# Kernel tuning notes

Measured on AMD Instinct MI355X. Metric: run time of the kernel, lower is better.

## Reference

```python
import jax, jax.numpy as jnp
import numpy as np

PH, PW = 7, 7          # output_size
GRID = 2               # sampling_ratio
SCALES = (0.25, 0.125, 0.0625, 0.03125)  # 2^round(log2(feat/img)) per level
LVL_MIN, LVL_MAX = 2, 5                  # -log2(scales[0]), -log2(scales[-1])
CANON_SCALE, CANON_LVL = 224.0, 4.0
EPS = 1e-6


def setup_inputs() -> dict:
    key = jax.random.key(0)
    ks = jax.random.split(key, 6)
    B, C = 2, 256
    sizes = [(200, 200), (100, 100), (50, 50), (25, 25)]
    inp = {f"feat{i}": jax.random.normal(ks[i], (B, C, h, w), jnp.float32)
           for i, (h, w) in enumerate(sizes)}
    Nb = 256
    # boxes in 800x800 image coords, x1y1 + positive wh so 0<=x1<x2, 0<=y1<y2
    xy = jax.random.uniform(ks[4], (B, Nb, 2), jnp.float32, 0.0, 700.0)
    wh = jax.random.uniform(ks[5], (B, Nb, 2), jnp.float32, 32.0, 512.0)
    inp["boxes"] = jnp.concatenate([xy, xy + wh], axis=-1)
    return inp


def _roi_align_level(feat, b_idx, rois, scale):
    """torchvision roi_align, aligned=False. feat [B,C,H,W], rois [R,4] -> [R,C,PH,PW]."""
    H, W = feat.shape[2], feat.shape[3]
    x1 = rois[:, 0] * scale
    y1 = rois[:, 1] * scale
    x2 = rois[:, 2] * scale
    y2 = rois[:, 3] * scale
    roi_w = jnp.maximum(x2 - x1, 1.0)
    roi_h = jnp.maximum(y2 - y1, 1.0)
    bin_w = roi_w / PW
    bin_h = roi_h / PH
    # sub-bin sampling offsets: (bin + (i+0.5)/grid) for each bin, flattened [PH*GRID]
    gy = (jnp.arange(PH, dtype=jnp.float32)[:, None]
          + (jnp.arange(GRID, dtype=jnp.float32)[None, :] + 0.5) / GRID).reshape(-1)
    gx = (jnp.arange(PW, dtype=jnp.float32)[:, None]
          + (jnp.arange(GRID, dtype=jnp.float32)[None, :] + 0.5) / GRID).reshape(-1)
    ys = y1[:, None] + gy[None, :] * bin_h[:, None]   # [R, PH*G]
    xs = x1[:, None] + gx[None, :] * bin_w[:, None]   # [R, PW*G]
    y = ys[:, :, None]                                 # [R, PH*G, 1]
    x = xs[:, None, :]                                 # [R, 1, PW*G]
    valid = (y >= -1.0) & (y <= H) & (x >= -1.0) & (x <= W)
    yc = jnp.clip(y, 0.0, H - 1)
    xc = jnp.clip(x, 0.0, W - 1)
    yl = jnp.floor(yc).astype(jnp.int32)
    xl = jnp.floor(xc).astype(jnp.int32)
    yh = jnp.minimum(yl + 1, H - 1)
    xh = jnp.minimum(xl + 1, W - 1)
    ly = yc - yl.astype(yc.dtype)
    lx = xc - xl.astype(xc.dtype)
    hy = 1.0 - ly
    hx = 1.0 - lx
    b = b_idx[:, None, None]

    def gather(yi, xi):
        # advanced indexing with slice in channel dim -> [R, PH*G, PW*G, C]
        return feat[b, :, yi, xi]

    val = ((hy * hx)[..., None] * gather(yl, xl)
           + (hy * lx)[..., None] * gather(yl, xh)
           + (ly * hx)[..., None] * gather(yh, xl)
           + (ly * lx)[..., None] * gather(yh, xh))
    val = jnp.where(valid[..., None], val, 0.0)
    R, C = rois.shape[0], feat.shape[1]
    # average over the GRIDxGRID sampling points of each bin
    val = val.reshape(R, PH, GRID, PW, GRID, C).mean(axis=(2, 4))  # [R,PH,PW,C]
    return jnp.transpose(val, (0, 3, 1, 2))                        # [R,C,PH,PW]


def reference(feat0, feat1, feat2, feat3, boxes):
    feats = [feat0, feat1, feat2, feat3]
    B, Nb = boxes.shape[0], boxes.shape[1]
    rois = boxes.reshape(-1, 4)                               # convert_to_roi_format
    b_idx = jnp.repeat(jnp.arange(B), Nb)
    # LevelMapper (FPN eq. 1)
    s = jnp.sqrt(jnp.maximum((rois[:, 2] - rois[:, 0]) * (rois[:, 3] - rois[:, 1]), 0.0))
    lvl = jnp.floor(CANON_LVL + jnp.log2(s / CANON_SCALE + EPS))
    lvl = jnp.clip(lvl, LVL_MIN, LVL_MAX).astype(jnp.int32) - LVL_MIN  # [R] in [0,3]
    out = jnp.zeros((rois.shape[0], feats[0].shape[1], PH, PW), feats[0].dtype)
    for l, (f, sc) in enumerate(zip(feats, SCALES)):
        pooled = _roi_align_level(f, b_idx, rois, sc)
        out = jnp.where((lvl == l)[:, None, None, None], pooled, out)
    return out
```

## Files before the change

### kernel.cpp

```cpp
#include <hip/hip_runtime.h>


#define PHW 49
#define NCHUNK 8
#define CH 32
#define PSIZE 1024

__global__ __launch_bounds__(64) void msroi_kernel(
    const float* __restrict__ f0, const float* __restrict__ f1,
    const float* __restrict__ f2, const float* __restrict__ f3,
    const float* __restrict__ boxes, float* __restrict__ out)
{
    const int C = 256, Nb = 256;
    const int r = blockIdx.x;
    const int chunk = blockIdx.y;
    const int tid = threadIdx.x;
    const int b = r / Nb;

    const float x1b = boxes[r * 4 + 0];
    const float y1b = boxes[r * 4 + 1];
    const float x2b = boxes[r * 4 + 2];
    const float y2b = boxes[r * 4 + 3];
    const float area = fmaxf((x2b - x1b) * (y2b - y1b), 0.0f);
    const float s = sqrtf(area);
    float lv = floorf(4.0f + log2f(s / 224.0f + 1e-6f));
    lv = fminf(fmaxf(lv, 2.0f), 5.0f);
    const int lvl = (int)lv - 2;

    const float* feat;
    int H, W;
    float scale;
    switch (lvl) {
        case 0:  feat = f0; H = 200; W = 200; scale = 0.25f;    break;
        case 1:  feat = f1; H = 100; W = 100; scale = 0.125f;   break;
        case 2:  feat = f2; H = 50;  W = 50;  scale = 0.0625f;  break;
        default: feat = f3; H = 25;  W = 25;  scale = 0.03125f; break;
    }
    const int HW = H * W;

    const float x1 = x1b * scale, y1 = y1b * scale;
    const float x2 = x2b * scale, y2 = y2b * scale;
    const float roi_w = fmaxf(x2 - x1, 1.0f);
    const float roi_h = fmaxf(y2 - y1, 1.0f);
    const float bin_w = roi_w * (1.0f / 7.0f);
    const float bin_h = roi_h * (1.0f / 7.0f);

    const float ys0 = fminf(fmaxf(y1 + 0.25f * bin_h, 0.0f), (float)(H - 1));
    const float ys1 = fminf(fmaxf(y1 + 6.75f * bin_h, 0.0f), (float)(H - 1));
    const float xs0 = fminf(fmaxf(x1 + 0.25f * bin_w, 0.0f), (float)(W - 1));
    const float xs1 = fminf(fmaxf(x1 + 6.75f * bin_w, 0.0f), (float)(W - 1));
    const int row0 = (int)floorf(ys0);
    const int row1 = min((int)floorf(ys1) + 1, H - 1);
    const int col0 = (int)floorf(xs0);
    const int col1 = min((int)floorf(xs1) + 1, W - 1);
    const int prows = row1 - row0 + 1;
    const int pcols = col1 - col0 + 1;
    const int psize = prows * pcols;
    const int wstride = W - pcols;
    const float inv_pcols = 1.0f / (float)pcols;

    int goff[16];
#pragma unroll
    for (int k = 0; k < 16; ++k) {
        const int e = tid + k * 64;
        const int ec = min(e, psize - 1);
        const int rr = (int)floorf(((float)ec + 0.5f) * inv_pcols);
        goff[k] = ec + rr * wstride;
    }
    const int kmax = (psize + 63) >> 6;

    const int bin = tid;
    const bool active = bin < PHW;
    int   offs[16];
    float wts[16];
    {
        const int bb = active ? bin : 0;
        const int ph = bb / 7;
        const int pw = bb - ph * 7;
#pragma unroll
        for (int g = 0; g < 4; ++g) {
            const int iy = g >> 1, ix = g & 1;
            const float gy = (float)ph + ((float)iy + 0.5f) * 0.5f;
            const float gx = (float)pw + ((float)ix + 0.5f) * 0.5f;
            const float y = y1 + gy * bin_h;
            const float x = x1 + gx * bin_w;
            const bool valid = (y >= -1.0f) && (y <= (float)H) &&
                               (x >= -1.0f) && (x <= (float)W);
            const float yc = fminf(fmaxf(y, 0.0f), (float)(H - 1));
            const float xc = fminf(fmaxf(x, 0.0f), (float)(W - 1));
            const int yl = (int)floorf(yc);
            const int xl = (int)floorf(xc);
            const int yh = min(yl + 1, H - 1);
            const int xh = min(xl + 1, W - 1);
            const float ly = yc - (float)yl;
            const float lx = xc - (float)xl;
            const float hy = 1.0f - ly, hx = 1.0f - lx;
            const float m = valid ? 0.25f : 0.0f;
            const int ry0 = (yl - row0) * pcols, ry1 = (yh - row0) * pcols;
            const int cx0 = xl - col0, cx1 = xh - col0;
            offs[g * 4 + 0] = ry0 + cx0;  wts[g * 4 + 0] = hy * hx * m;
            offs[g * 4 + 1] = ry0 + cx1;  wts[g * 4 + 1] = hy * lx * m;
            offs[g * 4 + 2] = ry1 + cx0;  wts[g * 4 + 2] = ly * hx * m;
            offs[g * 4 + 3] = ry1 + cx1;  wts[g * 4 + 3] = ly * lx * m;
        }
    }

    __shared__ float4 lds4[PSIZE];

    const int cbase = chunk * CH;
    const float* __restrict__ fch =
        feat + (size_t)(b * C + cbase) * HW + (row0 * W + col0);
    float* __restrict__ outp =
        out + (size_t)r * C * PHW + (size_t)cbase * PHW + bin;

    float4 buf[16];

#define LOADR(CCV)                                                         \
    do {                                                                   \
        const float* __restrict__ g0 = fch + (size_t)((CCV) + 0) * HW;     \
        const float* __restrict__ g1 = fch + (size_t)((CCV) + 1) * HW;     \
        const float* __restrict__ g2 = fch + (size_t)((CCV) + 2) * HW;     \
        const float* __restrict__ g3 = fch + (size_t)((CCV) + 3) * HW;     \
        _Pragma("unroll")                                                  \
        for (int k = 0; k < 16; ++k) {                                     \
            if (k < kmax) {       \
                buf[k].x = g0[goff[k]];                                    \
                buf[k].y = g1[goff[k]];                                    \
                buf[k].z = g2[goff[k]];                                    \
                buf[k].w = g3[goff[k]];                                    \
            }                                                              \
        }                                                                  \
    } while (0)

    LOADR(0);
    for (int cc = 0; cc < CH; cc += 4) {
        __syncthreads();
#pragma unroll
        for (int k = 0; k < 16; ++k)
            if (k < kmax) lds4[tid + k * 64] = buf[k];
        __syncthreads();

        if (cc + 4 < CH) LOADR(cc + 4);

        if (active) {
            float4 acc = make_float4(0.0f, 0.0f, 0.0f, 0.0f);
#pragma unroll
            for (int j = 0; j < 16; ++j) {
                const float4 v = lds4[offs[j]];
                acc.x += wts[j] * v.x;
                acc.y += wts[j] * v.y;
                acc.z += wts[j] * v.z;
                acc.w += wts[j] * v.w;
            }
            outp[(size_t)(cc + 0) * PHW] = acc.x;
            outp[(size_t)(cc + 1) * PHW] = acc.y;
            outp[(size_t)(cc + 2) * PHW] = acc.z;
            outp[(size_t)(cc + 3) * PHW] = acc.w;
        }
    }
#undef LOADR
}

extern "C" void kernel_launch(void* const* d_in, const int* in_sizes, int n_in,
                              void* d_out, int out_size, void* d_ws, size_t ws_size,
                              hipStream_t stream) {
    const float* f0 = (const float*)d_in[0];
    const float* f1 = (const float*)d_in[1];
    const float* f2 = (const float*)d_in[2];
    const float* f3 = (const float*)d_in[3];
    const float* boxes = (const float*)d_in[4];
    float* out = (float*)d_out;

    const int R = in_sizes[4] / 4;
    dim3 grid(R, NCHUNK);
    msroi_kernel<<<grid, 64, 0, stream>>>(f0, f1, f2, f3, boxes, out);
}
```

Before: 219.9 us.

## Split each bin's sampling points across four lanes with 256-thread blocks

```diff
diff --git a/kernel.cpp b/kernel.cpp
--- a/kernel.cpp
+++ b/kernel.cpp
@@ -6,7 +6,7 @@
 #define CH 32
 #define PSIZE 1024
 
-__global__ __launch_bounds__(64) void msroi_kernel(
+__global__ __launch_bounds__(256) void msroi_kernel(
     const float* __restrict__ f0, const float* __restrict__ f1,
     const float* __restrict__ f2, const float* __restrict__ f3,
     const float* __restrict__ boxes, float* __restrict__ out)
@@ -16,6 +16,10 @@
     const int chunk = blockIdx.y;
     const int tid = threadIdx.x;
     const int b = r / Nb;
+
+    const int bin = tid >> 2;
+    const int q   = tid & 3;
+    const bool active = bin < PHW;
 
     const float x1b = boxes[r * 4 + 0];
     const float y1b = boxes[r * 4 + 1];
@@ -59,50 +63,45 @@
     const int wstride = W - pcols;
     const float inv_pcols = 1.0f / (float)pcols;
 
-    int goff[16];
+    int goff[4];
 #pragma unroll
-    for (int k = 0; k < 16; ++k) {
-        const int e = tid + k * 64;
+    for (int k = 0; k < 4; ++k) {
+        const int e = tid + k * 256;
         const int ec = min(e, psize - 1);
         const int rr = (int)floorf(((float)ec + 0.5f) * inv_pcols);
         goff[k] = ec + rr * wstride;
     }
-    const int kmax = (psize + 63) >> 6;
+    const int kmax = (psize + 255) >> 8;
 
-    const int bin = tid;
-    const bool active = bin < PHW;
-    int   offs[16];
-    float wts[16];
+    int   offs[4];
+    float wts[4];
     {
         const int bb = active ? bin : 0;
         const int ph = bb / 7;
         const int pw = bb - ph * 7;
-#pragma unroll
-        for (int g = 0; g < 4; ++g) {
-            const int iy = g >> 1, ix = g & 1;
-            const float gy = (float)ph + ((float)iy + 0.5f) * 0.5f;
-            const float gx = (float)pw + ((float)ix + 0.5f) * 0.5f;
-            const float y = y1 + gy * bin_h;
-            const float x = x1 + gx * bin_w;
-            const bool valid = (y >= -1.0f) && (y <= (float)H) &&
-                               (x >= -1.0f) && (x <= (float)W);
-            const float yc = fminf(fmaxf(y, 0.0f), (float)(H - 1));
-            const float xc = fminf(fmaxf(x, 0.0f), (float)(W - 1));
-            const int yl = (int)floorf(yc);
-            const int xl = (int)floorf(xc);
-            const int yh = min(yl + 1, H - 1);
-            const int xh = min(xl + 1, W - 1);
-            const float ly = yc - (float)yl;
-            const float lx = xc - (float)xl;
-            const float hy = 1.0f - ly, hx = 1.0f - lx;
-            const float m = valid ? 0.25f : 0.0f;
-            const int ry0 = (yl - row0) * pcols, ry1 = (yh - row0) * pcols;
-            const int cx0 = xl - col0, cx1 = xh - col0;
-            offs[g * 4 + 0] = ry0 + cx0;  wts[g * 4 + 0] = hy * hx * m;
-            offs[g * 4 + 1] = ry0 + cx1;  wts[g * 4 + 1] = hy * lx * m;
-            offs[g * 4 + 2] = ry1 + cx0;  wts[g * 4 + 2] = ly * hx * m;
-            offs[g * 4 + 3] = ry1 + cx1;  wts[g * 4 + 3] = ly * lx * m;
-        }
+        const int iy = q >> 1, ix = q & 1;
+        const float gy = (float)ph + ((float)iy + 0.5f) * 0.5f;
+        const float gx = (float)pw + ((float)ix + 0.5f) * 0.5f;
+        const float y = y1 + gy * bin_h;
+        const float x = x1 + gx * bin_w;
+        const bool valid = (y >= -1.0f) && (y <= (float)H) &&
+                           (x >= -1.0f) && (x <= (float)W);
+        const float yc = fminf(fmaxf(y, 0.0f), (float)(H - 1));
+        const float xc = fminf(fmaxf(x, 0.0f), (float)(W - 1));
+        const int yl = (int)floorf(yc);
+        const int xl = (int)floorf(xc);
+        const int yh = min(yl + 1, H - 1);
+        const int xh = min(xl + 1, W - 1);
+        const float ly = yc - (float)yl;
+        const float lx = xc - (float)xl;
+        const float hy = 1.0f - ly, hx = 1.0f - lx;
+        const float m = valid ? 0.25f : 0.0f;
+        const int ry0 = (yl - row0) * pcols, ry1 = (yh - row0) * pcols;
+        const int cx0 = xl - col0, cx1 = xh - col0;
+        offs[0] = ry0 + cx0;  wts[0] = hy * hx * m;
+        offs[1] = ry0 + cx1;  wts[1] = hy * lx * m;
+        offs[2] = ry1 + cx0;  wts[2] = ly * hx * m;
+        offs[3] = ry1 + cx1;  wts[3] = ly * lx * m;
     }
 
     __shared__ float4 lds4[PSIZE];
@@ -111,9 +110,9 @@
     const float* __restrict__ fch =
         feat + (size_t)(b * C + cbase) * HW + (row0 * W + col0);
     float* __restrict__ outp =
-        out + (size_t)r * C * PHW + (size_t)cbase * PHW + bin;
+        out + (size_t)r * C * PHW + (size_t)cbase * PHW;
 
-    float4 buf[16];
+    float4 buf[4];
 
 #define LOADR(CCV)                                                         \
     do {                                                                   \
@@ -122,7 +121,7 @@
         const float* __restrict__ g2 = fch + (size_t)((CCV) + 2) * HW;     \
         const float* __restrict__ g3 = fch + (size_t)((CCV) + 3) * HW;     \
         _Pragma("unroll")                                                  \
-        for (int k = 0; k < 16; ++k) {                                     \
+        for (int k = 0; k < 4; ++k) {                                      \
             if (k < kmax) {       \
                 buf[k].x = g0[goff[k]];                                    \
                 buf[k].y = g1[goff[k]];                                    \
@@ -136,26 +135,29 @@
     for (int cc = 0; cc < CH; cc += 4) {
         __syncthreads();
 #pragma unroll
-        for (int k = 0; k < 16; ++k)
-            if (k < kmax) lds4[tid + k * 64] = buf[k];
+        for (int k = 0; k < 4; ++k)
+            if (k < kmax) lds4[tid + k * 256] = buf[k];
         __syncthreads();
 
         if (cc + 4 < CH) LOADR(cc + 4);
 
         if (active) {
-            float4 acc = make_float4(0.0f, 0.0f, 0.0f, 0.0f);
+            float4 a = make_float4(0.0f, 0.0f, 0.0f, 0.0f);
 #pragma unroll
-            for (int j = 0; j < 16; ++j) {
+            for (int j = 0; j < 4; ++j) {
                 const float4 v = lds4[offs[j]];
-                acc.x += wts[j] * v.x;
-                acc.y += wts[j] * v.y;
-                acc.z += wts[j] * v.z;
-                acc.w += wts[j] * v.w;
+                a.x += wts[j] * v.x;
+                a.y += wts[j] * v.y;
+                a.z += wts[j] * v.z;
+                a.w += wts[j] * v.w;
             }
-            outp[(size_t)(cc + 0) * PHW] = acc.x;
-            outp[(size_t)(cc + 1) * PHW] = acc.y;
-            outp[(size_t)(cc + 2) * PHW] = acc.z;
-            outp[(size_t)(cc + 3) * PHW] = acc.w;
+            a.x += __shfl_xor(a.x, 1); a.y += __shfl_xor(a.y, 1);
+            a.z += __shfl_xor(a.z, 1); a.w += __shfl_xor(a.w, 1);
+            a.x += __shfl_xor(a.x, 2); a.y += __shfl_xor(a.y, 2);
+            a.z += __shfl_xor(a.z, 2); a.w += __shfl_xor(a.w, 2);
+            const float vout = (q == 0) ? a.x : (q == 1) ? a.y
+                             : (q == 2) ? a.z : a.w;
+            outp[(size_t)(cc + q) * PHW + bin] = vout;
         }
     }
 #undef LOADR
@@ -173,5 +175,5 @@
 
     const int R = in_sizes[4] / 4;
     dim3 grid(R, NCHUNK);
-    msroi_kernel<<<grid, 64, 0, stream>>>(f0, f1, f2, f3, boxes, out);
+    msroi_kernel<<<grid, 256, 0, stream>>>(f0, f1, f2, f3, boxes, out);
 }
```

Result: faster. 180.8 us (-17.8%).
